# Kernel tuning notes

Hardware: AMD Instinct MI355X
Metric: run time of the kernel (lower is better)

The kernel has to match this reference:

```python
import jax, jax.numpy as jnp
import numpy as np

C = 128
K = 5
M = 150000   # num vertices
NF = 300000  # num faces
D = 192      # volume side
NEG_SLOPE = 0.2


def _x_shift(K):
    # Exactly replicates the torch module's grid construction.
    grid = np.linspace(-K // 2, K // 2, K)
    grid_3d = np.stack(np.meshgrid(grid, grid, grid), axis=0).transpose(2, 1, 3, 0)
    return jnp.asarray(grid_3d.reshape(-1, 3), jnp.float32)  # [K^3, 3]


def _trilinear_border(vol, g):
    # vol: [D1, D2, D3]; g: [N, 3] normalized coords in (x, y, z) order
    # (x -> D3/W, y -> D2/H, z -> D1/D), align_corners=True, padding_mode='border'.
    D1, D2, D3 = vol.shape
    def pix(c, S):
        return jnp.clip((c + 1.0) * 0.5 * (S - 1), 0.0, S - 1.0)
    ix, iy, iz = pix(g[:, 0], D3), pix(g[:, 1], D2), pix(g[:, 2], D1)
    x0f, y0f, z0f = jnp.floor(ix), jnp.floor(iy), jnp.floor(iz)
    wx, wy, wz = ix - x0f, iy - y0f, iz - z0f
    x0 = x0f.astype(jnp.int32); y0 = y0f.astype(jnp.int32); z0 = z0f.astype(jnp.int32)
    x1 = jnp.minimum(x0 + 1, D3 - 1)
    y1 = jnp.minimum(y0 + 1, D2 - 1)
    z1 = jnp.minimum(z0 + 1, D1 - 1)
    c000 = vol[z0, y0, x0]; c001 = vol[z0, y0, x1]
    c010 = vol[z0, y1, x0]; c011 = vol[z0, y1, x1]
    c100 = vol[z1, y0, x0]; c101 = vol[z1, y0, x1]
    c110 = vol[z1, y1, x0]; c111 = vol[z1, y1, x1]
    c00 = c000 * (1 - wx) + c001 * wx
    c01 = c010 * (1 - wx) + c011 * wx
    c10 = c100 * (1 - wx) + c101 * wx
    c11 = c110 * (1 - wx) + c111 * wx
    c0 = c00 * (1 - wy) + c01 * wy
    c1 = c10 * (1 - wy) + c11 * wy
    return c0 * (1 - wz) + c1 * wz


def _leaky(x):
    return jnp.where(x >= 0, x, NEG_SLOPE * x)


def setup_inputs() -> dict:
    key = jax.random.key(0)
    ks = jax.random.split(key, 9)
    v = jax.random.uniform(ks[0], (1, M, 3), jnp.float32, -0.9, 0.9)
    f = jax.random.randint(ks[1], (1, NF, 3), 0, M, jnp.int32)
    V = jax.random.normal(ks[2], (1, 1, D, D, D), jnp.float32)
    def init(k, shape, fan):
        return jax.random.normal(k, shape, jnp.float32) / np.sqrt(fan).astype(np.float32)
    Wconv = init(ks[3], (C, 1, K, K, K), K ** 3)
    bconv = jnp.zeros((C,), jnp.float32)
    Wlfc = init(ks[4], (C, C), C)
    blfc = jnp.zeros((C,), jnp.float32)
    W1 = init(ks[5], (C, 6), 6)
    b1 = jnp.zeros((C,), jnp.float32)
    W2 = init(ks[6], (4 * C, 2 * C), 2 * C)
    b2 = jnp.zeros((4 * C,), jnp.float32)
    W3 = init(ks[7], (2 * C, 4 * C), 4 * C)
    b3 = jnp.zeros((2 * C,), jnp.float32)
    return dict(v=v, f=f, V=V, Wconv=Wconv, bconv=bconv, Wlfc=Wlfc, blfc=blfc,
                W1=W1, b1=b1, W2=W2, b2=b2, W3=W3, b3=b3)


def reference(v, f, V, Wconv, bconv, Wlfc, blfc, W1, b1, W2, b2, W3, b3):
    m = v.shape[1]
    D1, D2, D3 = V.shape[2], V.shape[3], V.shape[4]
    Dm = max(D1, D2, D3)
    rescale = jnp.array([D3 / Dm, D2 / Dm, D1 / Dm], jnp.float32)
    x_shift = _x_shift(K)  # [K^3, 3]

    # --- cube sampling (Q = n_scale = 1), done under no_grad in torch ---
    pts = (v[0][:, None, :] + x_shift / Dm * 2.0) / rescale  # [m, K^3, 3]
    cubes = _trilinear_border(V[0, 0], pts.reshape(-1, 3)).reshape(m, K ** 3)
    cubes = jax.lax.stop_gradient(cubes)

    # --- localconv: Conv3d with full-size kernel == GEMM over flattened cube ---
    z_local = cubes @ Wconv.reshape(C, -1).T + bconv      # [m, C]
    z_local = _leaky(z_local)
    z_local = _leaky(z_local @ Wlfc.T + blfc)             # [m, C]

    # --- vertex normals (area-weighted face-normal accumulation, pytorch3d style) ---
    faces = f[0]
    vv = v[0]
    p0, p1, p2 = vv[faces[:, 0]], vv[faces[:, 1]], vv[faces[:, 2]]
    fn = jnp.cross(p1 - p0, p2 - p0)
    vn = jnp.zeros_like(vv)
    vn = vn.at[faces[:, 0]].add(fn).at[faces[:, 1]].add(fn).at[faces[:, 2]].add(fn)
    vn = vn / jnp.maximum(jnp.linalg.norm(vn, axis=-1, keepdims=True), 1e-6)

    # --- point-wise MLP fusion ---
    x = jnp.concatenate([v, vn[None]], axis=2)            # [1, m, 6]
    z_point = _leaky(x @ W1.T + b1)                       # [1, m, C]
    z = jnp.concatenate([z_point, z_local[None]], axis=2) # [1, m, 2C]
    z = _leaky(z @ W2.T + b2)                             # [1, m, 4C]
    z = _leaky(z @ W3.T + b3)                             # [1, m, 2C]
    return z
```

## Files before the change

kernel.cpp:

```cpp
#include <hip/hip_runtime.h>
#include <hip/hip_fp16.h>

#define NEG_SLOPE 0.2f

using f16x8 = __attribute__((ext_vector_type(8))) _Float16;
using f32x4 = __attribute__((ext_vector_type(4))) float;

__device__ __forceinline__ float leakyf(float x) { return x >= 0.f ? x : NEG_SLOPE * x; }

__device__ __forceinline__ void gload_lds16(const void* g, void* l) {
    __builtin_amdgcn_global_load_lds(
        (const __attribute__((address_space(1))) unsigned int*)g,
        (__attribute__((address_space(3))) unsigned int*)l, 16, 0, 0);
}

__global__ __launch_bounds__(256)
void normals_kernel(const float* __restrict__ v, const int* __restrict__ f,
                    float* __restrict__ vn, int nf) {
    int i = blockIdx.x * 256 + threadIdx.x;
    if (i >= nf) return;
    int i0 = f[3 * i], i1 = f[3 * i + 1], i2 = f[3 * i + 2];
    float p0x = v[3 * i0], p0y = v[3 * i0 + 1], p0z = v[3 * i0 + 2];
    float ux = v[3 * i1] - p0x, uy = v[3 * i1 + 1] - p0y, uz = v[3 * i1 + 2] - p0z;
    float wx = v[3 * i2] - p0x, wy = v[3 * i2 + 1] - p0y, wz = v[3 * i2 + 2] - p0z;
    float fx = uy * wz - uz * wy;
    float fy = uz * wx - ux * wz;
    float fz = ux * wy - uy * wx;
    atomicAdd(&vn[3 * i0 + 0], fx); atomicAdd(&vn[3 * i0 + 1], fy); atomicAdd(&vn[3 * i0 + 2], fz);
    atomicAdd(&vn[3 * i1 + 0], fx); atomicAdd(&vn[3 * i1 + 1], fy); atomicAdd(&vn[3 * i1 + 2], fz);
    atomicAdd(&vn[3 * i2 + 0], fx); atomicAdd(&vn[3 * i2 + 1], fy); atomicAdd(&vn[3 * i2 + 2], fz);
}

__global__ __launch_bounds__(256)
void sample_kernel(const float* __restrict__ v, const float* __restrict__ vol,
                   __half* __restrict__ cubes, int m_start, int cnt) {
    int tid = blockIdx.x * 256 + threadIdx.x;
    int ml = tid >> 7, q = tid & 127;
    if (ml >= cnt) return;
    __half* dst = cubes + (size_t)ml * 128;
    if (q >= 125) { dst[q] = __float2half(0.f); return; }
    int a = q % 5, b = (q / 5) % 5, c = q / 25;
    int m = m_start + ml;
    float ga = -3.f + 1.25f * (float)a;
    float gb = -3.f + 1.25f * (float)b;
    float gc = -3.f + 1.25f * (float)c;
    float px = v[3 * m + 0] + ga / 192.f * 2.f;
    float py = v[3 * m + 1] + gb / 192.f * 2.f;
    float pz = v[3 * m + 2] + gc / 192.f * 2.f;
    float ix = fminf(fmaxf((px + 1.f) * 0.5f * 191.f, 0.f), 191.f);
    float iy = fminf(fmaxf((py + 1.f) * 0.5f * 191.f, 0.f), 191.f);
    float iz = fminf(fmaxf((pz + 1.f) * 0.5f * 191.f, 0.f), 191.f);
    float xf = floorf(ix), yf = floorf(iy), zf = floorf(iz);
    float wxv = ix - xf, wyv = iy - yf, wzv = iz - zf;
    int x0 = (int)xf, y0 = (int)yf, z0 = (int)zf;
    int x1 = min(x0 + 1, 191), y1 = min(y0 + 1, 191), z1 = min(z0 + 1, 191);
    const float* pz0y0 = vol + z0 * 36864 + y0 * 192;
    const float* pz0y1 = vol + z0 * 36864 + y1 * 192;
    const float* pz1y0 = vol + z1 * 36864 + y0 * 192;
    const float* pz1y1 = vol + z1 * 36864 + y1 * 192;
    float c000 = pz0y0[x0], c001 = pz0y0[x1];
    float c010 = pz0y1[x0], c011 = pz0y1[x1];
    float c100 = pz1y0[x0], c101 = pz1y0[x1];
    float c110 = pz1y1[x0], c111 = pz1y1[x1];
    float omx = 1.f - wxv, omy = 1.f - wyv, omz = 1.f - wzv;
    float c00 = c000 * omx + c001 * wxv;
    float c01 = c010 * omx + c011 * wxv;
    float c10 = c100 * omx + c101 * wxv;
    float c11 = c110 * omx + c111 * wxv;
    float c0 = c00 * omy + c01 * wyv;
    float c1 = c10 * omy + c11 * wyv;
    dst[25 * a + 5 * b + c] = __float2half(c0 * omz + c1 * wzv);
}

__global__ __launch_bounds__(256)
void prep_weights(const float* __restrict__ Wconv, const float* __restrict__ Wlfc,
                  const float* __restrict__ W2, const float* __restrict__ W3,
                  __half* __restrict__ wpadh, __half* __restrict__ wlfch,
                  __half* __restrict__ w2h, __half* __restrict__ w3h) {
    int b = blockIdx.x, t = threadIdx.x;
    if (b < 64) {
        int i = b * 256 + t; int ch = i >> 7, k = i & 127;
        wpadh[i] = __float2half(k < 125 ? Wconv[ch * 125 + k] : 0.f);
    } else if (b < 128) {
        int i = (b - 64) * 256 + t; wlfch[i] = __float2half(Wlfc[i]);
    } else if (b < 640) {
        int i = (b - 128) * 256 + t; w2h[i] = __float2half(W2[i]);
    } else {
        int i = (b - 640) * 256 + t; w3h[i] = __float2half(W3[i]);
    }
}

__global__ __launch_bounds__(256)
void point_kernel(const float* __restrict__ v, const float* __restrict__ vn,
                  const float* __restrict__ W1, const float* __restrict__ b1,
                  __half* __restrict__ zcat, int m_start, int cnt) {
    int ml = blockIdx.x * 2 + (threadIdx.x >> 7);
    if (ml >= cnt) return;
    int n = threadIdx.x & 127;
    int m = m_start + ml;
    float x0 = v[3 * m], x1 = v[3 * m + 1], x2 = v[3 * m + 2];
    float nx = vn[3 * m], ny = vn[3 * m + 1], nz = vn[3 * m + 2];
    float nrm = fmaxf(sqrtf(nx * nx + ny * ny + nz * nz), 1e-6f);
    nx /= nrm; ny /= nrm; nz /= nrm;
    const float* w = W1 + n * 6;
    float z = b1[n] + x0 * w[0] + x1 * w[1] + x2 * w[2] + nx * w[3] + ny * w[4] + nz * w[5];
    zcat[(size_t)ml * 256 + n] = __float2half(leakyf(z));
}

template<bool F32OUT>
__global__ __launch_bounds__(256)
void gemm_mfma(const __half* __restrict__ A, const __half* __restrict__ W,
               const float* __restrict__ bias, void* __restrict__ outp,
               int K, int Meff, int OS, int OC) {
    __shared__ __half As[8192];
    __shared__ __half Bs[8192];
    const int t = threadIdx.x;
    const int lane = t & 63, wave = t >> 6;
    const int lr = lane & 15, lg = lane >> 4;
    const int wm = wave >> 1, wn = wave & 1;
    const int m0 = blockIdx.x * 128, n0 = blockIdx.y * 128;

    const int srow = t >> 3;
    const int scb = ((t & 7) << 4) ^ (((t >> 3) & 7) << 4);
    const __half* Ag = A + (size_t)(m0 + srow) * K + (scb >> 1);
    const __half* Wg = W + (size_t)(n0 + srow) * K + (scb >> 1);
    __half* Al = As + wave * 512;
    __half* Bl = Bs + wave * 512;

    const int swz = (lr & 7) << 4;
    const char* aB = (const char*)As + (wm * 64 + lr) * 128;
    const char* bB = (const char*)Bs + (wn * 64 + lr) * 128;
    const int k0 = (lg * 16) ^ swz;
    const int k1 = (64 + lg * 16) ^ swz;

    f32x4 acc[4][4] = {};

    for (int kc = 0; kc < K; kc += 64) {
#pragma unroll
        for (int i = 0; i < 4; ++i) {
            gload_lds16(Ag + (size_t)i * 32 * K + kc, Al + i * 2048);
            gload_lds16(Wg + (size_t)i * 32 * K + kc, Bl + i * 2048);
        }
        __syncthreads();
        f16x8 af[4], bf[4];
#pragma unroll
        for (int fx = 0; fx < 4; ++fx) {
            af[fx] = *(const f16x8*)(aB + fx * 2048 + k0);
            bf[fx] = *(const f16x8*)(bB + fx * 2048 + k0);
        }
#pragma unroll
        for (int fm = 0; fm < 4; ++fm)
#pragma unroll
            for (int fn = 0; fn < 4; ++fn)
                acc[fm][fn] = __builtin_amdgcn_mfma_f32_16x16x32_f16(af[fm], bf[fn], acc[fm][fn], 0, 0, 0);
#pragma unroll
        for (int fx = 0; fx < 4; ++fx) {
            af[fx] = *(const f16x8*)(aB + fx * 2048 + k1);
            bf[fx] = *(const f16x8*)(bB + fx * 2048 + k1);
        }
#pragma unroll
        for (int fm = 0; fm < 4; ++fm)
#pragma unroll
            for (int fn = 0; fn < 4; ++fn)
                acc[fm][fn] = __builtin_amdgcn_mfma_f32_16x16x32_f16(af[fm], bf[fn], acc[fm][fn], 0, 0, 0);
        __syncthreads();
    }

    float bv[4];
#pragma unroll
    for (int fn = 0; fn < 4; ++fn) bv[fn] = bias[n0 + wn * 64 + fn * 16 + lr];
    const int rbase = m0 + wm * 64 + lg * 4;
    const int cbase = OC + n0 + wn * 64 + lr;
#pragma unroll
    for (int fm = 0; fm < 4; ++fm) {
#pragma unroll
        for (int r = 0; r < 4; ++r) {
            int row = rbase + fm * 16 + r;
            if (row < Meff) {
#pragma unroll
                for (int fn = 0; fn < 4; ++fn) {
                    float val = leakyf(acc[fm][fn][r] + bv[fn]);
                    if (F32OUT)
                        ((float*)outp)[(size_t)row * OS + cbase + fn * 16] = val;
                    else
                        ((__half*)outp)[(size_t)row * OS + cbase + fn * 16] = __float2half(val);
                }
            }
        }
    }
}

extern "C" void kernel_launch(void* const* d_in, const int* in_sizes, int n_in,
                              void* d_out, int out_size, void* d_ws, size_t ws_size,
                              hipStream_t stream) {
    const float* v = (const float*)d_in[0];
    const int* f = (const int*)d_in[1];
    const float* vol = (const float*)d_in[2];
    const float* Wconv = (const float*)d_in[3];
    const float* bconv = (const float*)d_in[4];
    const float* Wlfc = (const float*)d_in[5];
    const float* blfc = (const float*)d_in[6];
    const float* W1 = (const float*)d_in[7];
    const float* b1 = (const float*)d_in[8];
    const float* W2 = (const float*)d_in[9];
    const float* b2 = (const float*)d_in[10];
    const float* W3 = (const float*)d_in[11];
    const float* b3 = (const float*)d_in[12];
    float* out = (float*)d_out;
    const int M = in_sizes[0] / 3;
    const int NF = in_sizes[1] / 3;

    char* base = (char*)d_ws;
    float* vn = (float*)base;
    size_t off = ((size_t)M * 12 + 255) & ~(size_t)255;
    __half* wpadh = (__half*)(base + off); off += 32768;
    __half* wlfch = (__half*)(base + off); off += 32768;
    __half* w2h = (__half*)(base + off); off += 262144;
    __half* w3h = (__half*)(base + off); off += 262144;
    size_t avail = ws_size > off ? ws_size - off : 0;
    size_t Mpad = ((size_t)M + 127) & ~(size_t)127;
    size_t chm = (avail / 2048) & ~(size_t)127;
    if (chm > Mpad) chm = Mpad;
    if (chm < 128) chm = 128;
    __half* cubes = (__half*)(base + off);
    __half* z0 = cubes + chm * 128;
    __half* zcat = z0 + chm * 128;
    __half* h = zcat + chm * 256;

    hipMemsetAsync(vn, 0, (size_t)M * 12, stream);
    normals_kernel<<<(NF + 255) / 256, 256, 0, stream>>>(v, f, vn, NF);
    prep_weights<<<1152, 256, 0, stream>>>(Wconv, Wlfc, W2, W3, wpadh, wlfch, w2h, w3h);

    for (size_t ms = 0; ms < (size_t)M; ms += chm) {
        size_t rem = (size_t)M - ms;
        int cnt = (int)(rem < chm ? rem : chm);
        int mb = (cnt + 127) / 128;
        sample_kernel<<<(cnt * 128 + 255) / 256, 256, 0, stream>>>(v, vol, cubes, (int)ms, cnt);
        gemm_mfma<false><<<dim3(mb, 1), 256, 0, stream>>>(cubes, wpadh, bconv, z0, 128, mb * 128, 128, 0);
        gemm_mfma<false><<<dim3(mb, 1), 256, 0, stream>>>(z0, wlfch, blfc, zcat, 128, mb * 128, 256, 128);
        point_kernel<<<(cnt + 1) / 2, 256, 0, stream>>>(v, vn, W1, b1, zcat, (int)ms, cnt);
        gemm_mfma<false><<<dim3(mb, 4), 256, 0, stream>>>(zcat, w2h, b2, h, 256, mb * 128, 512, 0);
        gemm_mfma<true><<<dim3(mb, 2), 256, 0, stream>>>(h, w3h, b3, out + ms * 256, 512, cnt, 256, 0);
    }
}
```

Measured before the change: 558.3 us.

## Sort vertices by Morton code for locality in volume sampling, scatter outputs back

Adds a 4096-bin Morton-code counting sort (histogram, scan, scatter) so vertices are processed in spatial order. The sample and point kernels read vertices through the permutation, and the final GEMM scatters rows back to their original positions. The aim is better cache reuse of the trilinear volume gathers. The sample kernel also remaps block IDs so that contiguous blocks land on the same XCD. The cost is three extra small kernels, a memset, and scattered, row-indirect output writes.

New measurement: 617.3 us. +10.6%, slower.

```diff
diff --git a/kernel.cpp b/kernel.cpp
--- a/kernel.cpp
+++ b/kernel.cpp
@@ -32,15 +32,66 @@
 }
 
 __global__ __launch_bounds__(256)
+void code_hist_kernel(const float* __restrict__ v, int* __restrict__ codes,
+                      int* __restrict__ hist, int M) {
+    int i = blockIdx.x * 256 + threadIdx.x;
+    if (i >= M) return;
+    int cx = min(max((int)((v[3 * i + 0] + 1.f) * 8.f), 0), 15);
+    int cy = min(max((int)((v[3 * i + 1] + 1.f) * 8.f), 0), 15);
+    int cz = min(max((int)((v[3 * i + 2] + 1.f) * 8.f), 0), 15);
+    int code = 0;
+#pragma unroll
+    for (int b = 0; b < 4; ++b)
+        code |= (((cx >> b) & 1) << (3 * b)) | (((cy >> b) & 1) << (3 * b + 1)) |
+                (((cz >> b) & 1) << (3 * b + 2));
+    codes[i] = code;
+    atomicAdd(&hist[code], 1);
+}
+
+__global__ __launch_bounds__(1024)
+void scan_kernel(const int* __restrict__ hist, int* __restrict__ offs) {
+    __shared__ int s[1024];
+    int t = threadIdx.x;
+    int v0 = hist[4 * t], v1 = hist[4 * t + 1], v2 = hist[4 * t + 2], v3 = hist[4 * t + 3];
+    int sum = v0 + v1 + v2 + v3;
+    s[t] = sum;
+    __syncthreads();
+    for (int d = 1; d < 1024; d <<= 1) {
+        int val = (t >= d) ? s[t - d] : 0;
+        __syncthreads();
+        s[t] += val;
+        __syncthreads();
+    }
+    int excl = s[t] - sum;
+    offs[4 * t + 0] = excl;
+    offs[4 * t + 1] = excl + v0;
+    offs[4 * t + 2] = excl + v0 + v1;
+    offs[4 * t + 3] = excl + v0 + v1 + v2;
+}
+
+__global__ __launch_bounds__(256)
+void scatter_kernel(const int* __restrict__ codes, int* __restrict__ offs,
+                    int* __restrict__ perm, int M) {
+    int i = blockIdx.x * 256 + threadIdx.x;
+    if (i >= M) return;
+    int pos = atomicAdd(&offs[codes[i]], 1);
+    perm[pos] = i;
+}
+
+__global__ __launch_bounds__(256)
 void sample_kernel(const float* __restrict__ v, const float* __restrict__ vol,
-                   __half* __restrict__ cubes, int m_start, int cnt) {
-    int tid = blockIdx.x * 256 + threadIdx.x;
+                   const int* __restrict__ perm,
+                   __half* __restrict__ cubes, int m_start, int cnt, int nwg) {
+    int q8 = nwg >> 3, r8 = nwg & 7;
+    int xcd = blockIdx.x & 7, idx = blockIdx.x >> 3;
+    int bid = (xcd < r8 ? xcd * (q8 + 1) : r8 * (q8 + 1) + (xcd - r8) * q8) + idx;
+    int tid = bid * 256 + threadIdx.x;
     int ml = tid >> 7, q = tid & 127;
     if (ml >= cnt) return;
     __half* dst = cubes + (size_t)ml * 128;
     if (q >= 125) { dst[q] = __float2half(0.f); return; }
     int a = q % 5, b = (q / 5) % 5, c = q / 25;
-    int m = m_start + ml;
+    int m = perm[m_start + ml];
     float ga = -3.f + 1.25f * (float)a;
     float gb = -3.f + 1.25f * (float)b;
     float gc = -3.f + 1.25f * (float)c;
@@ -92,12 +143,13 @@
 
 __global__ __launch_bounds__(256)
 void point_kernel(const float* __restrict__ v, const float* __restrict__ vn,
+                  const int* __restrict__ perm,
                   const float* __restrict__ W1, const float* __restrict__ b1,
                   __half* __restrict__ zcat, int m_start, int cnt) {
     int ml = blockIdx.x * 2 + (threadIdx.x >> 7);
     if (ml >= cnt) return;
     int n = threadIdx.x & 127;
-    int m = m_start + ml;
+    int m = perm[m_start + ml];
     float x0 = v[3 * m], x1 = v[3 * m + 1], x2 = v[3 * m + 2];
     float nx = vn[3 * m], ny = vn[3 * m + 1], nz = vn[3 * m + 2];
     float nrm = fmaxf(sqrtf(nx * nx + ny * ny + nz * nz), 1e-6f);
@@ -111,7 +163,7 @@
 __global__ __launch_bounds__(256)
 void gemm_mfma(const __half* __restrict__ A, const __half* __restrict__ W,
                const float* __restrict__ bias, void* __restrict__ outp,
-               int K, int Meff, int OS, int OC) {
+               int K, int Meff, int OS, int OC, const int* __restrict__ rowmap) {
     __shared__ __half As[8192];
     __shared__ __half Bs[8192];
     const int t = threadIdx.x;
@@ -177,13 +229,14 @@
         for (int r = 0; r < 4; ++r) {
             int row = rbase + fm * 16 + r;
             if (row < Meff) {
+                size_t orow = (size_t)(rowmap ? rowmap[row] : row);
 #pragma unroll
                 for (int fn = 0; fn < 4; ++fn) {
                     float val = leakyf(acc[fm][fn][r] + bv[fn]);
                     if (F32OUT)
-                        ((float*)outp)[(size_t)row * OS + cbase + fn * 16] = val;
+                        ((float*)outp)[orow * OS + cbase + fn * 16] = val;
                     else
-                        ((__half*)outp)[(size_t)row * OS + cbase + fn * 16] = __float2half(val);
+                        ((__half*)outp)[orow * OS + cbase + fn * 16] = __float2half(val);
                 }
             }
         }
@@ -213,6 +266,10 @@
     char* base = (char*)d_ws;
     float* vn = (float*)base;
     size_t off = ((size_t)M * 12 + 255) & ~(size_t)255;
+    int* codes = (int*)(base + off); off += ((size_t)M * 4 + 255) & ~(size_t)255;
+    int* perm  = (int*)(base + off); off += ((size_t)M * 4 + 255) & ~(size_t)255;
+    int* hist  = (int*)(base + off); off += 4096 * 4;
+    int* offs  = (int*)(base + off); off += 4096 * 4;
     __half* wpadh = (__half*)(base + off); off += 32768;
     __half* wlfch = (__half*)(base + off); off += 32768;
     __half* w2h = (__half*)(base + off); off += 262144;
@@ -228,18 +285,23 @@
     __half* h = zcat + chm * 256;
 
     hipMemsetAsync(vn, 0, (size_t)M * 12, stream);
+    hipMemsetAsync(hist, 0, 4096 * 4, stream);
     normals_kernel<<<(NF + 255) / 256, 256, 0, stream>>>(v, f, vn, NF);
+    code_hist_kernel<<<(M + 255) / 256, 256, 0, stream>>>(v, codes, hist, M);
+    scan_kernel<<<1, 1024, 0, stream>>>(hist, offs);
+    scatter_kernel<<<(M + 255) / 256, 256, 0, stream>>>(codes, offs, perm, M);
     prep_weights<<<1152, 256, 0, stream>>>(Wconv, Wlfc, W2, W3, wpadh, wlfch, w2h, w3h);
 
     for (size_t ms = 0; ms < (size_t)M; ms += chm) {
         size_t rem = (size_t)M - ms;
         int cnt = (int)(rem < chm ? rem : chm);
         int mb = (cnt + 127) / 128;
-        sample_kernel<<<(cnt * 128 + 255) / 256, 256, 0, stream>>>(v, vol, cubes, (int)ms, cnt);
-        gemm_mfma<false><<<dim3(mb, 1), 256, 0, stream>>>(cubes, wpadh, bconv, z0, 128, mb * 128, 128, 0);
-        gemm_mfma<false><<<dim3(mb, 1), 256, 0, stream>>>(z0, wlfch, blfc, zcat, 128, mb * 128, 256, 128);
-        point_kernel<<<(cnt + 1) / 2, 256, 0, stream>>>(v, vn, W1, b1, zcat, (int)ms, cnt);
-        gemm_mfma<false><<<dim3(mb, 4), 256, 0, stream>>>(zcat, w2h, b2, h, 256, mb * 128, 512, 0);
-        gemm_mfma<true><<<dim3(mb, 2), 256, 0, stream>>>(h, w3h, b3, out + ms * 256, 512, cnt, 256, 0);
-    }
-}
+        int nwg = (cnt * 128 + 255) / 256;
+        sample_kernel<<<nwg, 256, 0, stream>>>(v, vol, perm, cubes, (int)ms, cnt, nwg);
+        gemm_mfma<false><<<dim3(mb, 1), 256, 0, stream>>>(cubes, wpadh, bconv, z0, 128, mb * 128, 128, 0, nullptr);
+        gemm_mfma<false><<<dim3(mb, 1), 256, 0, stream>>>(z0, wlfch, blfc, zcat, 128, mb * 128, 256, 128, nullptr);
+        point_kernel<<<(cnt + 1) / 2, 256, 0, stream>>>(v, vn, perm, W1, b1, zcat, (int)ms, cnt);
+        gemm_mfma<false><<<dim3(mb, 4), 256, 0, stream>>>(zcat, w2h, b2, h, 256, mb * 128, 512, 0, nullptr);
+        gemm_mfma<true><<<dim3(mb, 2), 256, 0, stream>>>(h, w3h, b3, out, 512, cnt, 256, 0, perm + ms);
+    }
+}
```
